# Kernel tuning notes

Hardware: AMD Instinct MI355X
Metric: run time of the kernel (lower is better)

## Reference

```python
import jax, jax.numpy as jnp
import numpy as np

FG_IOU = 0.7
BG_IOU = 0.3
IMG_H = 640.0
IMG_W = 640.0


def setup_inputs() -> dict:
    key = jax.random.key(0)
    k1, k2, k3, k4 = jax.random.split(key, 4)
    B, A, G = 8, 184320, 64
    # anchors in cxcywh (as the torch module assumes before box_convert)
    cxcy = jax.random.uniform(k1, (B, A, 2), dtype=jnp.float32) * 640.0
    wh = 16.0 + jax.random.uniform(k2, (B, A, 2), dtype=jnp.float32) * 240.0
    anchors = jnp.concatenate([cxcy, wh], axis=-1)
    # gt boxes in xyxy, inside the 640x640 image
    xy1 = jax.random.uniform(k3, (B, G, 2), dtype=jnp.float32) * 560.0
    wh_g = 24.0 + jax.random.uniform(k4, (B, G, 2), dtype=jnp.float32) * 180.0
    gt_boxes = jnp.concatenate([xy1, jnp.minimum(xy1 + wh_g, 640.0)], axis=-1)
    return {"anchors": anchors, "gt_boxes": gt_boxes}


def cxcywh_to_xyxy(b):
    cx, cy, w, h = b[..., 0], b[..., 1], b[..., 2], b[..., 3]
    return jnp.stack([cx - 0.5 * w, cy - 0.5 * h, cx + 0.5 * w, cy + 0.5 * h], axis=-1)


def box_iou(a, g):
    # a: [A,4] xyxy, g: [G,4] xyxy -> [A,G]
    area_a = (a[:, 2] - a[:, 0]) * (a[:, 3] - a[:, 1])
    area_g = (g[:, 2] - g[:, 0]) * (g[:, 3] - g[:, 1])
    lt = jnp.maximum(a[:, None, :2], g[None, :, :2])   # [A,G,2]
    rb = jnp.minimum(a[:, None, 2:], g[None, :, 2:])
    wh = jnp.clip(rb - lt, 0.0)
    inter = wh[..., 0] * wh[..., 1]
    return inter / (area_a[:, None] + area_g[None, :] - inter)


def _assign_one(anchors_cxcywh, gt):
    # anchors_cxcywh: [A,4], gt: [G,4] xyxy
    A = anchors_cxcywh.shape[0]
    a = cxcywh_to_xyxy(anchors_cxcywh)                 # [A,4]
    iou = box_iou(a, gt)                               # [A,G]

    labels = jnp.full((A,), -1, dtype=jnp.int32)
    matched = jnp.zeros((A, 4), dtype=anchors_cxcywh.dtype)

    # rule 1: for each gt, the anchor attaining its max IoU is positive
    best_anchor = jnp.argmax(iou, axis=0)              # [G]
    labels = labels.at[best_anchor].set(1)
    matched = matched.at[best_anchor].set(gt)

    # rule 2: anchors with max IoU over gts > fg threshold are positive
    max_gt = jnp.argmax(iou, axis=1)                   # [A]
    max_val = jnp.max(iou, axis=1)                     # [A]
    fg = max_val > FG_IOU
    labels = jnp.where(fg, 1, labels)
    matched = jnp.where(fg[:, None], gt[max_gt], matched)

    # rule 3: remaining anchors with max IoU < bg threshold are negative
    bg = (max_val < BG_IOU) & (labels < 0)
    labels = jnp.where(bg, 0, labels)

    # filter cross-boundary anchors -> ignore label
    cross = (a[:, 0] < 0) | (a[:, 1] < 0) | (a[:, 2] > IMG_W) | (a[:, 3] > IMG_H)
    labels = jnp.where(cross, -1, labels)
    return labels, matched, max_val


def reference(anchors, gt_boxes):
    # anchors: [B,A,4] cxcywh, gt_boxes: [B,G,4] xyxy
    labels, matched_bboxes, max_iou = jax.vmap(_assign_one)(anchors, gt_boxes)
    return labels, matched_bboxes, max_iou
```

## Files before the change

kernel.cpp:

```cpp
#include <hip/hip_runtime.h>


constexpr int B = 8;
constexpr int G = 64;
constexpr int BLOCK = 256;
constexpr int APT = 2;
constexpr int ABLK = BLOCK * APT;
constexpr int NSTRIP = 128;
constexpr float STRIP_SCALE = 0.2f;
constexpr float STRIP_W = 5.0f;
constexpr float IMG = 640.0f;
constexpr float FG_IOU = 0.7f;
constexpr float BG_IOU = 0.3f;
constexpr float SLACK = 1.0f;
constexpr unsigned long long KEY_INIT = 0xFFFFFFFFull;


__global__ __launch_bounds__(512) void build_tables(
    const float4* __restrict__ gt, unsigned long long* __restrict__ tabs) {
    __shared__ float4 sgt[G];
    const int b = blockIdx.x;
    const int t = threadIdx.x;
    if (t < G) sgt[t] = gt[b * G + t];
    __syncthreads();
    const int tabIdx = t >> 7;
    const int strip = t & 127;
    const int comp = (tabIdx == 0) ? 0 : (tabIdx == 1) ? 2 : (tabIdx == 2) ? 1 : 3;
    const bool hi = (tabIdx & 1) != 0;
    const float thr = hi ? (strip * STRIP_W - SLACK)
                         : ((strip + 1) * STRIP_W + SLACK);
    unsigned long long m = 0ull;
    for (int g = 0; g < G; ++g) {
        float c = ((const float*)&sgt[g])[comp];
        bool in = hi ? (c > thr) : (c < thr);
        if (in) m |= (1ull << g);
    }
    tabs[(size_t)b * 512 + t] = m;
}

__global__ __launch_bounds__(BLOCK) void assign_main(
    const float4* __restrict__ anchors,
    const float4* __restrict__ gt,
    float* __restrict__ L,
    float4* __restrict__ M,
    float* __restrict__ V,
    long long* __restrict__ gkeys,
    const unsigned long long* __restrict__ tabs,
    int A, int bpb) {
#pragma clang fp contract(off)
    __shared__ float sgx0[G], sgy0[G], sgx1[G], sgy1[G], sga[G];
    __shared__ unsigned long long tab[4][NSTRIP];
    __shared__ unsigned long long skey[G];

    const int b = blockIdx.x / bpb;
    const int t = threadIdx.x;
    const int base = (blockIdx.x % bpb) * ABLK;

    if (t < G) {
        float4 gb = gt[b * G + t];
        sgx0[t] = gb.x; sgy0[t] = gb.y; sgx1[t] = gb.z; sgy1[t] = gb.w;
        sga[t] = (gb.z - gb.x) * (gb.w - gb.y);
        skey[t] = KEY_INIT;
    }
    {
        const ulonglong2* src = (const ulonglong2*)(tabs + (size_t)b * 512);
        ((ulonglong2*)&tab[0][0])[t] = src[t];
    }
    __syncthreads();

    const int a0 = base + t;
    const int a1 = base + BLOCK + t;
    const size_t idx0 = (size_t)b * A + a0;
    const size_t idx1 = (size_t)b * A + a1;
    const float4 anbuf[APT] = { anchors[idx0], anchors[idx1] };

#pragma unroll
    for (int j = 0; j < APT; ++j) {
        const int a = j == 0 ? a0 : a1;
        const size_t idx = j == 0 ? idx0 : idx1;
        const float4 an = anbuf[j];
        float ax0 = an.x - 0.5f * an.z;
        float ay0 = an.y - 0.5f * an.w;
        float ax1 = an.x + 0.5f * an.z;
        float ay1 = an.y + 0.5f * an.w;
        float area_a = (ax1 - ax0) * (ay1 - ay0);

        int sx0 = (int)(ax0 * STRIP_SCALE); sx0 = sx0 < 0 ? 0 : (sx0 > 127 ? 127 : sx0);
        int sx1 = (int)(ax1 * STRIP_SCALE); sx1 = sx1 < 0 ? 0 : (sx1 > 127 ? 127 : sx1);
        int sy0 = (int)(ay0 * STRIP_SCALE); sy0 = sy0 < 0 ? 0 : (sy0 > 127 ? 127 : sy0);
        int sy1 = (int)(ay1 * STRIP_SCALE); sy1 = sy1 < 0 ? 0 : (sy1 > 127 ? 127 : sy1);

        unsigned long long mask =
            tab[0][sx1] & tab[1][sx0] & tab[2][sy1] & tab[3][sy0];

        float maxv = 0.0f;
        int maxg = 0;
        const unsigned long long inv_p =
            (unsigned long long)(0xFFFFFFFFu - (unsigned)a);

        auto half = [&](unsigned m, int gbase) {
            if (!m) return;
            int g = gbase + __builtin_ctz(m);
            m &= m - 1;
            float gx0 = sgx0[g], gy0 = sgy0[g];
            float gx1 = sgx1[g], gy1 = sgy1[g];
            float sa = sga[g];
            for (;;) {
                const bool more = m != 0u;
                const int gn = gbase + __builtin_ctz(m | 0x80000000u);
                m &= m - 1;
                const float nx0 = sgx0[gn], ny0 = sgy0[gn];
                const float nx1 = sgx1[gn], ny1 = sgy1[gn];
                const float nsa = sga[gn];

                float lx = fmaxf(ax0, gx0);
                float ly = fmaxf(ay0, gy0);
                float rx = fminf(ax1, gx1);
                float ry = fminf(ay1, gy1);
                float w = fmaxf(rx - lx, 0.0f);
                float h = fmaxf(ry - ly, 0.0f);
                float inter = w * h;
                float uni = area_a + sa - inter;
                float iou = inter / uni;

                bool better = iou > maxv;
                maxv = better ? iou : maxv;
                maxg = better ? g : maxg;

                unsigned long long key =
                    ((unsigned long long)__float_as_uint(iou) << 32) | inv_p;
                atomicMax(&skey[g], key);

                if (!more) break;
                g = gn;
                gx0 = nx0; gy0 = ny0; gx1 = nx1; gy1 = ny1; sa = nsa;
            }
        };
        half((unsigned)mask, 0);
        half((unsigned)(mask >> 32), 32);

        bool fg = maxv > FG_IOU;
        bool bg = maxv < BG_IOU;
        bool cross = (ax0 < 0.0f) || (ay0 < 0.0f) || (ax1 > IMG) || (ay1 > IMG);

        L[idx] = cross ? -1.0f : (fg ? 1.0f : (bg ? 0.0f : -1.0f));
        float4 mbox = make_float4(0.0f, 0.0f, 0.0f, 0.0f);
        if (fg)
            mbox = make_float4(sgx0[maxg], sgy0[maxg], sgx1[maxg], sgy1[maxg]);
        M[idx] = mbox;
        V[idx] = maxv;
    }

    __syncthreads();
    if (t < G) {
        atomicMax(&gkeys[b * G + t], (long long)skey[t]);
    }
}

__global__ void fixup(
    const float4* __restrict__ anchors,
    const float4* __restrict__ gt,
    const long long* __restrict__ gkeys,
    float* __restrict__ L,
    float4* __restrict__ M,
    const float* __restrict__ V,
    int A) {
#pragma clang fp contract(off)
    const int b = blockIdx.x;
    const int g = threadIdx.x;
    __shared__ int tgt[G];

    unsigned long long key = (unsigned long long)gkeys[b * G + g];
    unsigned int a = 0xFFFFFFFFu - (unsigned int)(key & 0xFFFFFFFFull);
    tgt[g] = (int)a;
    __syncthreads();

    bool write = true;
    for (int g2 = g + 1; g2 < G; ++g2)
        if (tgt[g2] == (int)a) { write = false; break; }
    if (!write) return;

    const size_t idx = (size_t)b * A + a;
    float4 an = anchors[idx];
    float ax0 = an.x - 0.5f * an.z;
    float ay0 = an.y - 0.5f * an.w;
    float ax1 = an.x + 0.5f * an.z;
    float ay1 = an.y + 0.5f * an.w;
    bool cross = (ax0 < 0.0f) || (ay0 < 0.0f) || (ax1 > IMG) || (ay1 > IMG);
    L[idx] = cross ? -1.0f : 1.0f;
    if (!(V[idx] > FG_IOU)) M[idx] = gt[b * G + g];
}

extern "C" void kernel_launch(void* const* d_in, const int* in_sizes, int n_in,
                              void* d_out, int out_size, void* d_ws, size_t ws_size,
                              hipStream_t stream) {
    const float4* anchors = (const float4*)d_in[0];
    const float4* gt      = (const float4*)d_in[1];
    const int A = in_sizes[0] / (B * 4);

    float* out = (float*)d_out;
    float*  L = out;
    float4* M = (float4*)(out + (size_t)B * A);
    float*  V = out + (size_t)B * A * 5;

    char* ws = (char*)d_ws;
    long long* gkeys = (long long*)(ws + 256);
    unsigned long long* tabs = (unsigned long long*)(ws + 8192);

    const int bpb = A / ABLK;
    build_tables<<<B, 512, 0, stream>>>(gt, tabs);
    assign_main<<<B * bpb, BLOCK, 0, stream>>>(anchors, gt, L, M, V, gkeys,
                                               tabs, A, bpb);
    fixup<<<B, G, 0, stream>>>(anchors, gt, gkeys, L, M, V, A);
}
```

Before: 122.0 us.

## Load-balance anchor-gt IoU pairs via per-chunk shared work queue

Each anchor's candidate GT mask is compacted into a shared-memory queue of (anchor, gt) pairs per 128-anchor chunk. All 256 threads then process the queue evenly, instead of each thread looping over a variable number of candidates. Per-anchor max/argmax moves to 64-bit shared atomics keyed by IoU and inverted gt index, and anchors per thread go from 2 to 3. The aim is to cut warp divergence and load imbalance. The cost is extra block barriers, wave-wide prefix scans, more shared-memory atomics, and a larger shared footprint that may lower occupancy.

```diff
diff --git a/kernel.cpp b/kernel.cpp
--- a/kernel.cpp
+++ b/kernel.cpp
@@ -4,8 +4,11 @@
 constexpr int B = 8;
 constexpr int G = 64;
 constexpr int BLOCK = 256;
-constexpr int APT = 2;
+constexpr int APT = 3;
 constexpr int ABLK = BLOCK * APT;
+constexpr int CHUNK = 128;
+constexpr int NCHUNK = ABLK / CHUNK;
+constexpr int QCAP = CHUNK * G;
 constexpr int NSTRIP = 128;
 constexpr float STRIP_SCALE = 0.2f;
 constexpr float STRIP_W = 5.0f;
@@ -14,6 +17,7 @@
 constexpr float BG_IOU = 0.3f;
 constexpr float SLACK = 1.0f;
 constexpr unsigned long long KEY_INIT = 0xFFFFFFFFull;
+constexpr unsigned long long ROW_INIT = 63ull;
 
 
 __global__ __launch_bounds__(512) void build_tables(
@@ -51,10 +55,17 @@
     __shared__ float sgx0[G], sgy0[G], sgx1[G], sgy1[G], sga[G];
     __shared__ unsigned long long tab[4][NSTRIP];
     __shared__ unsigned long long skey[G];
+    __shared__ unsigned short queue[QCAP];
+    __shared__ float sax0[CHUNK], say0[CHUNK], sax1[CHUNK], say1[CHUNK],
+                     sarea[CHUNK];
+    __shared__ unsigned long long rowkey[CHUNK];
+    __shared__ int qcnt[NCHUNK];
 
     const int b = blockIdx.x / bpb;
     const int t = threadIdx.x;
     const int base = (blockIdx.x % bpb) * ABLK;
+    const int lane = t & 63;
+    const int tl = t & (CHUNK - 1);
 
     if (t < G) {
         float4 gb = gt[b * G + t];
@@ -62,93 +73,117 @@
         sga[t] = (gb.z - gb.x) * (gb.w - gb.y);
         skey[t] = KEY_INIT;
     }
+    if (t < NCHUNK) qcnt[t] = 0;
     {
         const ulonglong2* src = (const ulonglong2*)(tabs + (size_t)b * 512);
         ((ulonglong2*)&tab[0][0])[t] = src[t];
     }
-    __syncthreads();
-
-    const int a0 = base + t;
-    const int a1 = base + BLOCK + t;
-    const size_t idx0 = (size_t)b * A + a0;
-    const size_t idx1 = (size_t)b * A + a1;
-    const float4 anbuf[APT] = { anchors[idx0], anchors[idx1] };
-
+
+    float4 anbuf[NCHUNK];
 #pragma unroll
-    for (int j = 0; j < APT; ++j) {
-        const int a = j == 0 ? a0 : a1;
-        const size_t idx = j == 0 ? idx0 : idx1;
-        const float4 an = anbuf[j];
-        float ax0 = an.x - 0.5f * an.z;
-        float ay0 = an.y - 0.5f * an.w;
-        float ax1 = an.x + 0.5f * an.z;
-        float ay1 = an.y + 0.5f * an.w;
-        float area_a = (ax1 - ax0) * (ay1 - ay0);
+    for (int c = 0; c < NCHUNK; ++c)
+        anbuf[c] = anchors[(size_t)b * A + base + c * CHUNK + tl];
+
+    __syncthreads();
+
+#pragma unroll
+    for (int c = 0; c < NCHUNK; ++c) {
+        const float4 an = anbuf[c];
+        const float ax0 = an.x - 0.5f * an.z;
+        const float ay0 = an.y - 0.5f * an.w;
+        const float ax1 = an.x + 0.5f * an.z;
+        const float ay1 = an.y + 0.5f * an.w;
+        const float area_a = (ax1 - ax0) * (ay1 - ay0);
+
+        if (t < CHUNK) {
+            sax0[tl] = ax0; say0[tl] = ay0; sax1[tl] = ax1; say1[tl] = ay1;
+            sarea[tl] = area_a;
+            rowkey[tl] = ROW_INIT;
+        }
 
         int sx0 = (int)(ax0 * STRIP_SCALE); sx0 = sx0 < 0 ? 0 : (sx0 > 127 ? 127 : sx0);
         int sx1 = (int)(ax1 * STRIP_SCALE); sx1 = sx1 < 0 ? 0 : (sx1 > 127 ? 127 : sx1);
         int sy0 = (int)(ay0 * STRIP_SCALE); sy0 = sy0 < 0 ? 0 : (sy0 > 127 ? 127 : sy0);
         int sy1 = (int)(ay1 * STRIP_SCALE); sy1 = sy1 < 0 ? 0 : (sy1 > 127 ? 127 : sy1);
-
-        unsigned long long mask =
+        const unsigned long long mask =
             tab[0][sx1] & tab[1][sx0] & tab[2][sy1] & tab[3][sy0];
 
-        float maxv = 0.0f;
-        int maxg = 0;
-        const unsigned long long inv_p =
-            (unsigned long long)(0xFFFFFFFFu - (unsigned)a);
-
-        auto half = [&](unsigned m, int gbase) {
-            if (!m) return;
-            int g = gbase + __builtin_ctz(m);
-            m &= m - 1;
-            float gx0 = sgx0[g], gy0 = sgy0[g];
-            float gx1 = sgx1[g], gy1 = sgy1[g];
-            float sa = sga[g];
-            for (;;) {
-                const bool more = m != 0u;
-                const int gn = gbase + __builtin_ctz(m | 0x80000000u);
-                m &= m - 1;
-                const float nx0 = sgx0[gn], ny0 = sgy0[gn];
-                const float nx1 = sgx1[gn], ny1 = sgy1[gn];
-                const float nsa = sga[gn];
-
-                float lx = fmaxf(ax0, gx0);
-                float ly = fmaxf(ay0, gy0);
-                float rx = fminf(ax1, gx1);
-                float ry = fminf(ay1, gy1);
-                float w = fmaxf(rx - lx, 0.0f);
-                float h = fmaxf(ry - ly, 0.0f);
+        unsigned hm = (t < CHUNK) ? (unsigned)mask : (unsigned)(mask >> 32);
+        const int gb2 = (t < CHUNK) ? 0 : 32;
+        const int pop = __builtin_popcount(hm);
+
+        int x = pop;
+#pragma unroll
+        for (int d = 1; d < 64; d <<= 1) {
+            int y = __shfl_up(x, d, 64);
+            if (lane >= d) x += y;
+        }
+        int wbase = 0;
+        if (lane == 63) wbase = atomicAdd(&qcnt[c], x);
+        wbase = __shfl(wbase, 63, 64);
+        int p = wbase + x - pop;
+
+        while (hm) {
+            const int g = gb2 + (int)__builtin_ctz(hm);
+            hm &= hm - 1;
+            queue[p++] = (unsigned short)((tl << 6) | g);
+        }
+        __syncthreads();
+
+        const int nq = qcnt[c];
+        const int R = (nq + BLOCK - 1) >> 8;
+        const int Rp = R | 1;
+        const int ibase = t * Rp;
+
+        auto consume = [&](int i) {
+            if (i < nq) {
+                const int item = (int)queue[i];
+                const int al = item >> 6;
+                const int g = item & 63;
+                const float bx0 = sax0[al], by0 = say0[al];
+                const float bx1 = sax1[al], by1 = say1[al];
+                const float ba  = sarea[al];
+                const float gx0 = sgx0[g], gy0 = sgy0[g];
+                const float gx1 = sgx1[g], gy1 = sgy1[g];
+                const float ga  = sga[g];
+                float lx = fmaxf(bx0, gx0), ly = fmaxf(by0, gy0);
+                float rx = fminf(bx1, gx1), ry = fminf(by1, gy1);
+                float w = fmaxf(rx - lx, 0.0f), h = fmaxf(ry - ly, 0.0f);
                 float inter = w * h;
-                float uni = area_a + sa - inter;
+                float uni = ba + ga - inter;
                 float iou = inter / uni;
-
-                bool better = iou > maxv;
-                maxv = better ? iou : maxv;
-                maxg = better ? g : maxg;
-
-                unsigned long long key =
-                    ((unsigned long long)__float_as_uint(iou) << 32) | inv_p;
-                atomicMax(&skey[g], key);
-
-                if (!more) break;
-                g = gn;
-                gx0 = nx0; gy0 = ny0; gx1 = nx1; gy1 = ny1; sa = nsa;
+                const unsigned ag = (unsigned)(base + c * CHUNK + al);
+                const unsigned long long hi =
+                    (unsigned long long)__float_as_uint(iou) << 32;
+                atomicMax(&skey[g], hi | (unsigned long long)(0xFFFFFFFFu - ag));
+                atomicMax(&rowkey[al], hi | (unsigned long long)(63 - g));
             }
         };
-        half((unsigned)mask, 0);
-        half((unsigned)(mask >> 32), 32);
-
-        bool fg = maxv > FG_IOU;
-        bool bg = maxv < BG_IOU;
-        bool cross = (ax0 < 0.0f) || (ay0 < 0.0f) || (ax1 > IMG) || (ay1 > IMG);
-
-        L[idx] = cross ? -1.0f : (fg ? 1.0f : (bg ? 0.0f : -1.0f));
-        float4 mbox = make_float4(0.0f, 0.0f, 0.0f, 0.0f);
-        if (fg)
-            mbox = make_float4(sgx0[maxg], sgy0[maxg], sgx1[maxg], sgy1[maxg]);
-        M[idx] = mbox;
-        V[idx] = maxv;
+        for (int r = 0; r + 1 < Rp; r += 2) {
+            consume(ibase + r);
+            consume(ibase + r + 1);
+        }
+        consume(ibase + Rp - 1);
+        __syncthreads();
+
+        if (t < CHUNK) {
+            const unsigned long long key = rowkey[t];
+            const float maxv = __uint_as_float((unsigned)(key >> 32));
+            const int maxg = 63 - (int)(key & 0xFFFFFFFFull);
+            const float bx0 = sax0[t], by0 = say0[t];
+            const float bx1 = sax1[t], by1 = say1[t];
+            const bool fg = maxv > FG_IOU;
+            const bool bg = maxv < BG_IOU;
+            const bool cross =
+                (bx0 < 0.0f) || (by0 < 0.0f) || (bx1 > IMG) || (by1 > IMG);
+            const size_t idx = (size_t)b * A + (base + c * CHUNK + t);
+            L[idx] = cross ? -1.0f : (fg ? 1.0f : (bg ? 0.0f : -1.0f));
+            float4 mbox = make_float4(0.0f, 0.0f, 0.0f, 0.0f);
+            if (fg)
+                mbox = make_float4(sgx0[maxg], sgy0[maxg], sgx1[maxg], sgy1[maxg]);
+            M[idx] = mbox;
+            V[idx] = maxv;
+        }
     }
 
     __syncthreads();
```

Measured after the change: 130.9 us. +7.3%, slower.
